# Kernel tuning notes

Hardware: AMD Instinct MI355X
Metric: run time of the kernel (lower is better)

Reference implementation:

```python
import math
import jax, jax.numpy as jnp
import numpy as np

L, B, T, C, H = 12, 4, 1024, 1024, 16
D = C // H
EPS = 1e-5  # torch LayerNorm default


def setup_inputs() -> dict:
    key = jax.random.key(0)
    ks = jax.random.split(key, 8)
    s = 0.02
    return {
        "x": jax.random.normal(ks[0], (B, T, C), jnp.float32),
        "ln1_g": jnp.ones((L, C), jnp.float32),
        "ln1_b": jnp.zeros((L, C), jnp.float32),
        "attn_w": jax.random.normal(ks[1], (L, C, 3 * C), jnp.float32) * s,
        "attn_b": jnp.zeros((L, 3 * C), jnp.float32),
        "proj_w": jax.random.normal(ks[2], (L, C, C), jnp.float32) * s,
        "proj_b": jnp.zeros((L, C), jnp.float32),
        "ln2_g": jnp.ones((L, C), jnp.float32),
        "ln2_b": jnp.zeros((L, C), jnp.float32),
        "fc_w": jax.random.normal(ks[3], (L, C, 4 * C), jnp.float32) * s,
        "fc_b": jnp.zeros((L, 4 * C), jnp.float32),
        "fc2_w": jax.random.normal(ks[4], (L, 4 * C, C), jnp.float32) * s,
        "fc2_b": jnp.zeros((L, C), jnp.float32),
        "lnf_g": jnp.ones((C,), jnp.float32),
        "lnf_b": jnp.zeros((C,), jnp.float32),
    }


def layer_norm(x, g, b):
    m = jnp.mean(x, axis=-1, keepdims=True)
    v = jnp.var(x, axis=-1, keepdims=True)
    return (x - m) * jax.lax.rsqrt(v + EPS) * g + b


def new_gelu(x):
    # 0.5*x*(1+tanh(sqrt(2/pi)*(x+0.044715*x^3)))  (tanh-approx GELU)
    c = math.sqrt(2.0 / math.pi)
    return 0.5 * x * (1.0 + jnp.tanh(c * (x + 0.044715 * x ** 3)))


def block(x, p):
    ln1g, ln1b, aw, ab, pw, pb, ln2g, ln2b, fw, fb, f2w, f2b = p
    # causal self attention
    h = layer_norm(x, ln1g, ln1b)
    qkv = h @ aw + ab                                   # [B,T,3C]
    q, k, v = jnp.split(qkv, 3, axis=-1)
    q = q.reshape(B, T, H, D).transpose(0, 2, 1, 3)      # [B,H,T,D]
    k = k.reshape(B, T, H, D).transpose(0, 2, 1, 3)
    v = v.reshape(B, T, H, D).transpose(0, 2, 1, 3)
    att = jnp.einsum("bhqd,bhkd->bhqk", q, k) * (1.0 / math.sqrt(D))
    mask = jnp.tril(jnp.ones((T, T), dtype=bool))
    att = jnp.where(mask, att, -jnp.inf)
    att = jax.nn.softmax(att, axis=-1)
    y = jnp.einsum("bhqk,bhkd->bhqd", att, v)            # [B,H,T,D]
    y = y.transpose(0, 2, 1, 3).reshape(B, T, C)
    x = x + (y @ pw + pb)
    # MLP
    h = layer_norm(x, ln2g, ln2b)
    x = x + (new_gelu(h @ fw + fb) @ f2w + f2b)
    return x


def reference(x, ln1_g, ln1_b, attn_w, attn_b, proj_w, proj_b,
              ln2_g, ln2_b, fc_w, fc_b, fc2_w, fc2_b, lnf_g, lnf_b):
    params = (ln1_g, ln1_b, attn_w, attn_b, proj_w, proj_b,
              ln2_g, ln2_b, fc_w, fc_b, fc2_w, fc2_b)
    x, _ = jax.lax.scan(lambda c, p: (block(c, p), None), x, params)
    return layer_norm(x, lnf_g, lnf_b)
```

## Files before the change

kernel.cpp:

```cpp
#include <hip/hip_runtime.h>


typedef __bf16 bf16x8 __attribute__((ext_vector_type(8)));
typedef float f32x4 __attribute__((ext_vector_type(4)));
typedef unsigned short u16x8 __attribute__((ext_vector_type(8)));

__device__ __forceinline__ unsigned short f2b(float f) {
    union { float f; unsigned u; } x{f};
    unsigned r = x.u + 0x7FFF + ((x.u >> 16) & 1);
    return (unsigned short)(r >> 16);
}

__device__ __forceinline__ float gelu_f(float x) {
    float u = 0.7978845608028654f * (x + 0.044715f * x * x * x);
    float t = __expf(2.f * u);
    float th = 1.f - 2.f / (t + 1.f);
    return 0.5f * x * (1.f + th);
}

template <int BF16OUT>
__global__ __launch_bounds__(256) void ln_kernel(
    const float* __restrict__ x, const float* __restrict__ g,
    const float* __restrict__ bt, void* __restrict__ out) {
    const int row = blockIdx.x, tid = threadIdx.x;
    const float4 v = *(const float4*)(x + (size_t)row * 1024 + tid * 4);
    float s = v.x + v.y + v.z + v.w;
    float q = v.x * v.x + v.y * v.y + v.z * v.z + v.w * v.w;
    #pragma unroll
    for (int d = 1; d < 64; d <<= 1) { s += __shfl_xor(s, d); q += __shfl_xor(q, d); }
    __shared__ float ss[4], sq[4];
    const int w = tid >> 6;
    if ((tid & 63) == 0) { ss[w] = s; sq[w] = q; }
    __syncthreads();
    s = ss[0] + ss[1] + ss[2] + ss[3];
    q = sq[0] + sq[1] + sq[2] + sq[3];
    const float mean = s * (1.f / 1024.f);
    const float var = q * (1.f / 1024.f) - mean * mean;
    const float inv = rsqrtf(var + 1e-5f);
    const float4 gg = *(const float4*)(g + tid * 4);
    const float4 bb = *(const float4*)(bt + tid * 4);
    const float y0 = (v.x - mean) * inv * gg.x + bb.x;
    const float y1 = (v.y - mean) * inv * gg.y + bb.y;
    const float y2 = (v.z - mean) * inv * gg.z + bb.z;
    const float y3 = (v.w - mean) * inv * gg.w + bb.w;
    if (BF16OUT) {
        uint2 p;
        p.x = (unsigned)f2b(y0) | ((unsigned)f2b(y1) << 16);
        p.y = (unsigned)f2b(y2) | ((unsigned)f2b(y3) << 16);
        ((uint2*)out)[(size_t)row * 256 + tid] = p;
    } else {
        ((float4*)out)[(size_t)row * 256 + tid] = make_float4(y0, y1, y2, y3);
    }
}

__global__ __launch_bounds__(256) void wtrans_kernel(
    const float* __restrict__ W, unsigned short* __restrict__ Wt, int K, int N) {
    __shared__ float T[64][68];
    const int tid = threadIdx.x;
    const int n0 = blockIdx.x * 64, k0 = blockIdx.y * 64;
    #pragma unroll
    for (int r = 0; r < 4; ++r) {
        int li = tid + r * 256;
        int kk = li >> 4, nn = (li & 15) * 4;
        float4 v = *(const float4*)(W + (size_t)(k0 + kk) * N + n0 + nn);
        *(float4*)(&T[kk][nn]) = v;
    }
    __syncthreads();
    #pragma unroll
    for (int r = 0; r < 2; ++r) {
        int li = tid + r * 256;
        int nn = li >> 3, kc = li & 7;
        u16x8 t;
        #pragma unroll
        for (int j = 0; j < 8; ++j) t[j] = f2b(T[kc * 8 + j][nn]);
        *(u16x8*)(Wt + (size_t)(n0 + nn) * K + k0 + kc * 8) = t;
    }
}

template <int MODE>
__global__ __launch_bounds__(256) void gemm_kernel(
    const unsigned short* __restrict__ A, const unsigned short* __restrict__ Bt,
    const float* __restrict__ bias, const float* __restrict__ resid,
    void* __restrict__ out, int M, int N, int K) {
    __shared__ unsigned short As[128 * 72];
    __shared__ unsigned short Bs[128 * 72];
    const int tid = threadIdx.x, lane = tid & 63, w = tid >> 6;
    const int wm = w >> 1, wn = w & 1, lr = lane & 15, quad = lane >> 4;
    const int m0 = blockIdx.y * 128, n0 = blockIdx.x * 128;
    f32x4 acc[4][4] = {};
    const int nk = K >> 6;
    for (int kt = 0; kt < nk; ++kt) {
        #pragma unroll
        for (int r = 0; r < 4; ++r) {
            int ci = tid + r * 256;
            int row = ci >> 3, c = ci & 7;
            *(uint4*)(&As[row * 72 + c * 8]) =
                *(const uint4*)(A + (size_t)(m0 + row) * K + kt * 64 + c * 8);
            *(uint4*)(&Bs[row * 72 + c * 8]) =
                *(const uint4*)(Bt + (size_t)(n0 + row) * K + kt * 64 + c * 8);
        }
        __syncthreads();
        #pragma unroll
        for (int s = 0; s < 2; ++s) {
            bf16x8 af[4], bf[4];
            #pragma unroll
            for (int i = 0; i < 4; ++i)
                af[i] = *(const bf16x8*)(&As[(wm * 64 + i * 16 + lr) * 72 + s * 32 + quad * 8]);
            #pragma unroll
            for (int j = 0; j < 4; ++j)
                bf[j] = *(const bf16x8*)(&Bs[(wn * 64 + j * 16 + lr) * 72 + s * 32 + quad * 8]);
            #pragma unroll
            for (int i = 0; i < 4; ++i)
                #pragma unroll
                for (int j = 0; j < 4; ++j)
                    acc[i][j] = __builtin_amdgcn_mfma_f32_16x16x32_bf16(af[i], bf[j], acc[i][j], 0, 0, 0);
        }
        __syncthreads();
    }
    #pragma unroll
    for (int i = 0; i < 4; ++i) {
        #pragma unroll
        for (int j = 0; j < 4; ++j) {
            const int gm0 = m0 + wm * 64 + i * 16 + quad * 4;
            const int gn = n0 + wn * 64 + j * 16 + lr;
            const float bb = bias[gn];
            #pragma unroll
            for (int r = 0; r < 4; ++r) {
                float v = acc[i][j][r] + bb;
                const size_t idx = (size_t)(gm0 + r) * N + gn;
                if (MODE == 2) {
                    ((float*)out)[idx] = resid[idx] + v;
                } else {
                    if (MODE == 1) v = gelu_f(v);
                    ((unsigned short*)out)[idx] = f2b(v);
                }
            }
        }
    }
}

__global__ __launch_bounds__(256) void attn_kernel(
    const unsigned short* __restrict__ qkv, unsigned short* __restrict__ y) {
    __shared__ unsigned short Ks[64 * 64];
    __shared__ unsigned short Vt[64 * 64];
    __shared__ unsigned short Ps[4][16 * 64];
    const int tid = threadIdx.x, lane = tid & 63, w = tid >> 6;
    const int lr = lane & 15, quad = lane >> 4;
    const int bx = blockIdx.x, bh = blockIdx.y;
    const int b = bh >> 4, h = bh & 15;
    const int q0 = bx * 64;
    const unsigned short* base = qkv + (size_t)b * 1024 * 3072 + h * 64;

    bf16x8 qf[2];
    {
        const int qr = q0 + w * 16 + lr;
        qf[0] = *(const bf16x8*)(base + (size_t)qr * 3072 + quad * 8);
        qf[1] = *(const bf16x8*)(base + (size_t)qr * 3072 + 32 + quad * 8);
    }
    float m_r[4], l_r[4];
    f32x4 o[4] = {};
    #pragma unroll
    for (int r = 0; r < 4; ++r) { m_r[r] = -3e38f; l_r[r] = 0.f; }

    const int nkt = bx + 1;
    for (int kt = 0; kt < nkt; ++kt) {
        #pragma unroll
        for (int r2 = 0; r2 < 2; ++r2) {
            int ci = tid + r2 * 256;
            int kr = ci >> 3, c = ci & 7;
            uint4 v = *(const uint4*)(base + (size_t)(kt * 64 + kr) * 3072 + 1024 + c * 8);
            *(uint4*)(&Ks[kr * 64 + ((c ^ (kr & 7)) << 3)]) = v;
        }
        #pragma unroll
        for (int r2 = 0; r2 < 2; ++r2) {
            int vr = (tid >> 3) + r2 * 32;
            int c = (tid & 7) * 8;
            u16x8 v = *(const u16x8*)(base + (size_t)(kt * 64 + vr) * 3072 + 2048 + c);
            #pragma unroll
            for (int j = 0; j < 8; ++j) {
                int d = c + j;
                Vt[d * 64 + (((vr >> 3) ^ (d & 7)) << 3) + (vr & 7)] = v[j];
            }
        }
        __syncthreads();

        f32x4 sf[4];
        #pragma unroll
        for (int jk = 0; jk < 4; ++jk) {
            f32x4 cf = {};
            #pragma unroll
            for (int s = 0; s < 2; ++s) {
                int krow = jk * 16 + lr;
                bf16x8 kf = *(const bf16x8*)(&Ks[krow * 64 + ((((s << 2) + quad) ^ (krow & 7)) << 3)]);
                cf = __builtin_amdgcn_mfma_f32_16x16x32_bf16(qf[s], kf, cf, 0, 0, 0);
            }
            #pragma unroll
            for (int r = 0; r < 4; ++r) sf[jk][r] = cf[r] * 0.125f;
        }
        if (kt == bx) {
            #pragma unroll
            for (int jk = 0; jk < 4; ++jk)
                #pragma unroll
                for (int r = 0; r < 4; ++r) {
                    int kcol = q0 + jk * 16 + lr;
                    int qr = q0 + w * 16 + quad * 4 + r;
                    if (kcol > qr) sf[jk][r] = -3e38f;
                }
        }
        #pragma unroll
        for (int r = 0; r < 4; ++r) {
            float mx = fmaxf(fmaxf(sf[0][r], sf[1][r]), fmaxf(sf[2][r], sf[3][r]));
            #pragma unroll
            for (int d = 1; d < 16; d <<= 1) mx = fmaxf(mx, __shfl_xor(mx, d));
            const float mnew = fmaxf(m_r[r], mx);
            const float alpha = __expf(m_r[r] - mnew);
            float rs = 0.f;
            #pragma unroll
            for (int jk = 0; jk < 4; ++jk) {
                float p = __expf(sf[jk][r] - mnew);
                sf[jk][r] = p;
                rs += p;
            }
            #pragma unroll
            for (int d = 1; d < 16; d <<= 1) rs += __shfl_xor(rs, d);
            l_r[r] = l_r[r] * alpha + rs;
            m_r[r] = mnew;
            #pragma unroll
            for (int jd = 0; jd < 4; ++jd) o[jd][r] *= alpha;
        }
        #pragma unroll
        for (int jk = 0; jk < 4; ++jk)
            #pragma unroll
            for (int r = 0; r < 4; ++r) {
                int row = quad * 4 + r;
                int col = jk * 16 + lr;
                Ps[w][row * 64 + (((col >> 3) ^ (row & 7)) << 3) + (col & 7)] = f2b(sf[jk][r]);
            }
        __syncthreads();
        #pragma unroll
        for (int s2 = 0; s2 < 2; ++s2) {
            bf16x8 pf = *(const bf16x8*)(&Ps[w][lr * 64 + ((((s2 << 2) + quad) ^ (lr & 7)) << 3)]);
            #pragma unroll
            for (int jd = 0; jd < 4; ++jd) {
                int dr = jd * 16 + lr;
                bf16x8 vf = *(const bf16x8*)(&Vt[dr * 64 + ((((s2 << 2) + quad) ^ (dr & 7)) << 3)]);
                o[jd] = __builtin_amdgcn_mfma_f32_16x16x32_bf16(pf, vf, o[jd], 0, 0, 0);
            }
        }
        __syncthreads();
    }
    #pragma unroll
    for (int jd = 0; jd < 4; ++jd)
        #pragma unroll
        for (int r = 0; r < 4; ++r) {
            int qr = q0 + w * 16 + quad * 4 + r;
            int d = jd * 16 + lr;
            y[((size_t)b * 1024 + qr) * 1024 + h * 64 + d] = f2b(o[jd][r] / l_r[r]);
        }
}

extern "C" void kernel_launch(void* const* d_in, const int* in_sizes, int n_in,
                              void* d_out, int out_size, void* d_ws, size_t ws_size,
                              hipStream_t stream) {
    const float* x      = (const float*)d_in[0];
    const float* ln1_g  = (const float*)d_in[1];
    const float* ln1_b  = (const float*)d_in[2];
    const float* attn_w = (const float*)d_in[3];
    const float* attn_b = (const float*)d_in[4];
    const float* proj_w = (const float*)d_in[5];
    const float* proj_b = (const float*)d_in[6];
    const float* ln2_g  = (const float*)d_in[7];
    const float* ln2_b  = (const float*)d_in[8];
    const float* fc_w   = (const float*)d_in[9];
    const float* fc_b   = (const float*)d_in[10];
    const float* fc2_w  = (const float*)d_in[11];
    const float* fc2_b  = (const float*)d_in[12];
    const float* lnf_g  = (const float*)d_in[13];
    const float* lnf_b  = (const float*)d_in[14];

    char* ws = (char*)d_ws;
    float* xf            = (float*)ws;
    unsigned short* hbuf = (unsigned short*)(ws + (16u << 20));
    unsigned short* qkvb = (unsigned short*)(ws + (24u << 20));
    unsigned short* yb   = (unsigned short*)(ws + (48u << 20));
    unsigned short* h2   = (unsigned short*)(ws + (56u << 20));
    unsigned short* wq   = (unsigned short*)(ws + (88u << 20));
    unsigned short* wp   = (unsigned short*)(ws + (94u << 20));
    unsigned short* wf   = (unsigned short*)(ws + (96u << 20));
    unsigned short* wf2  = (unsigned short*)(ws + (104u << 20));

    hipMemcpyAsync(xf, x, (size_t)4096 * 1024 * 4, hipMemcpyDeviceToDevice, stream);

    for (int l = 0; l < 12; ++l) {
        wtrans_kernel<<<dim3(48, 16), 256, 0, stream>>>(attn_w + (size_t)l * 1024 * 3072, wq, 1024, 3072);
        wtrans_kernel<<<dim3(16, 16), 256, 0, stream>>>(proj_w + (size_t)l * 1024 * 1024, wp, 1024, 1024);
        wtrans_kernel<<<dim3(64, 16), 256, 0, stream>>>(fc_w + (size_t)l * 1024 * 4096, wf, 1024, 4096);
        wtrans_kernel<<<dim3(16, 64), 256, 0, stream>>>(fc2_w + (size_t)l * 4096 * 1024, wf2, 4096, 1024);

        ln_kernel<1><<<4096, 256, 0, stream>>>(xf, ln1_g + l * 1024, ln1_b + l * 1024, hbuf);
        gemm_kernel<0><<<dim3(24, 32), 256, 0, stream>>>(hbuf, wq, attn_b + l * 3072, nullptr,
                                                         qkvb, 4096, 3072, 1024);
        attn_kernel<<<dim3(16, 64), 256, 0, stream>>>(qkvb, yb);
        gemm_kernel<2><<<dim3(8, 32), 256, 0, stream>>>(yb, wp, proj_b + l * 1024, xf,
                                                        xf, 4096, 1024, 1024);
        ln_kernel<1><<<4096, 256, 0, stream>>>(xf, ln2_g + l * 1024, ln2_b + l * 1024, hbuf);
        gemm_kernel<1><<<dim3(32, 32), 256, 0, stream>>>(hbuf, wf, fc_b + l * 4096, nullptr,
                                                         h2, 4096, 4096, 1024);
        gemm_kernel<2><<<dim3(8, 32), 256, 0, stream>>>(h2, wf2, fc2_b + l * 1024, xf,
                                                        xf, 4096, 1024, 4096);
    }
    ln_kernel<0><<<4096, 256, 0, stream>>>(xf, lnf_g, lnf_b, d_out);
}
```

Baseline: 4.381 ms.

## Load GEMM tiles directly global-to-LDS with XOR-swizzled unpadded layout

```diff
diff --git a/kernel.cpp b/kernel.cpp
--- a/kernel.cpp
+++ b/kernel.cpp
@@ -16,6 +16,12 @@
     float t = __expf(2.f * u);
     float th = 1.f - 2.f / (t + 1.f);
     return 0.5f * x * (1.f + th);
+}
+
+__device__ __forceinline__ void g2l16(const unsigned short* g, unsigned short* l) {
+    __builtin_amdgcn_global_load_lds(
+        (const __attribute__((address_space(1))) void*)g,
+        (__attribute__((address_space(3))) void*)l, 16, 0, 0);
 }
 
 template <int BF16OUT>
@@ -82,33 +88,40 @@
     const unsigned short* __restrict__ A, const unsigned short* __restrict__ Bt,
     const float* __restrict__ bias, const float* __restrict__ resid,
     void* __restrict__ out, int M, int N, int K) {
-    __shared__ unsigned short As[128 * 72];
-    __shared__ unsigned short Bs[128 * 72];
+    __shared__ unsigned short As[128 * 64];
+    __shared__ unsigned short Bs[128 * 64];
     const int tid = threadIdx.x, lane = tid & 63, w = tid >> 6;
     const int wm = w >> 1, wn = w & 1, lr = lane & 15, quad = lane >> 4;
     const int m0 = blockIdx.y * 128, n0 = blockIdx.x * 128;
+
+    const int ar = lane >> 3;
+    const int ac = (lane & 7) ^ ar;
+    const unsigned short* Ag = A  + (size_t)(m0 + w * 32 + ar) * K + ac * 8;
+    const unsigned short* Bg = Bt + (size_t)(n0 + w * 32 + ar) * K + ac * 8;
+
     f32x4 acc[4][4] = {};
     const int nk = K >> 6;
     for (int kt = 0; kt < nk; ++kt) {
         #pragma unroll
         for (int r = 0; r < 4; ++r) {
-            int ci = tid + r * 256;
-            int row = ci >> 3, c = ci & 7;
-            *(uint4*)(&As[row * 72 + c * 8]) =
-                *(const uint4*)(A + (size_t)(m0 + row) * K + kt * 64 + c * 8);
-            *(uint4*)(&Bs[row * 72 + c * 8]) =
-                *(const uint4*)(Bt + (size_t)(n0 + row) * K + kt * 64 + c * 8);
-        }
+            g2l16(Ag + (size_t)(r * 8) * K, &As[(w * 32 + r * 8) * 64]);
+            g2l16(Bg + (size_t)(r * 8) * K, &Bs[(w * 32 + r * 8) * 64]);
+        }
+        Ag += 64; Bg += 64;
         __syncthreads();
         #pragma unroll
         for (int s = 0; s < 2; ++s) {
             bf16x8 af[4], bf[4];
             #pragma unroll
-            for (int i = 0; i < 4; ++i)
-                af[i] = *(const bf16x8*)(&As[(wm * 64 + i * 16 + lr) * 72 + s * 32 + quad * 8]);
-            #pragma unroll
-            for (int j = 0; j < 4; ++j)
-                bf[j] = *(const bf16x8*)(&Bs[(wn * 64 + j * 16 + lr) * 72 + s * 32 + quad * 8]);
+            for (int i = 0; i < 4; ++i) {
+                const int row = wm * 64 + i * 16 + lr;
+                af[i] = *(const bf16x8*)(&As[row * 64 + ((((s << 2) + quad) ^ (lr & 7)) << 3)]);
+            }
+            #pragma unroll
+            for (int j = 0; j < 4; ++j) {
+                const int row = wn * 64 + j * 16 + lr;
+                bf[j] = *(const bf16x8*)(&Bs[row * 64 + ((((s << 2) + quad) ^ (lr & 7)) << 3)]);
+            }
             #pragma unroll
             for (int i = 0; i < 4; ++i)
                 #pragma unroll
```

Result: no change. 4.377 ms (-0.1%).
